# Kernel tuning notes

Measured on AMD Instinct MI355X. Metric: run time of the kernel, lower is better.

## Reference

```python
import jax, jax.numpy as jnp
import numpy as np

B, N, D, H = 4, 4096, 1024, 16
DH = D // H            # 64
GH = 4 * DH            # gate hidden = 256
FREQ = N // 2 + 1      # 2049
INV_SQRT2 = 0.7071067811865476


def _ln(x, g, b, eps=1e-6):
    mu = jnp.mean(x, axis=-1, keepdims=True)
    var = jnp.mean((x - mu) ** 2, axis=-1, keepdims=True)
    return (x - mu) / jnp.sqrt(var + eps) * g + b


def _xavier(k, out_f, in_f, gain=0.8):
    bound = gain * (6.0 / (in_f + out_f)) ** 0.5
    return jax.random.uniform(k, (out_f, in_f), jnp.float32, -bound, bound)


def setup_inputs() -> dict:
    key = jax.random.key(0)
    ks = jax.random.split(key, 8)
    return {
        'x': jax.random.normal(ks[0], (B, N, D), jnp.float32),
        'Wq': _xavier(ks[1], D, D),
        'Wv': _xavier(ks[2], D, D),
        'Wo': _xavier(ks[3], D, D),
        'ln_g': jnp.ones((DH,), jnp.float32),
        'ln_b': jnp.zeros((DH,), jnp.float32),
        'Wgup': _xavier(ks[4], GH, DH),
        'Wgdn': _xavier(ks[5], 2 * FREQ, GH),
        'Wwup': _xavier(ks[6], GH, DH),
        'Wwdn': _xavier(ks[7], N, GH),
    }


def reference(x, Wq, Wv, Wo, ln_g, ln_b, Wgup, Wgdn, Wwup, Wwdn):
    Bx, Nx, Dx = x.shape
    # projections -> [B, H, N, DH]
    q = (x @ Wq.T).reshape(Bx, Nx, H, DH).transpose(0, 2, 1, 3)
    v = (x @ Wv.T).reshape(Bx, Nx, H, DH).transpose(0, 2, 1, 3)
    # per-head summary token -> complex spectral gate over FREQ bins
    bar = _ln(q.mean(axis=2), ln_g, ln_b)                    # [B, H, DH]
    gr = (jax.nn.silu(bar @ Wgup.T) @ Wgdn.T)               # [B, H, 2*FREQ]
    gr = gr.reshape(Bx, H, FREQ, 2)
    gate = jax.lax.complex(gr[..., 0], gr[..., 1])           # [B, H, FREQ]
    # spectral mixing (chunk == seq_len, power-of-two path)
    spec = jnp.fft.rfft(v, axis=2, norm='ortho') * gate[..., None]
    v_t = jnp.fft.irfft(spec, n=Nx, axis=2, norm='ortho')    # [B, H, N, DH]
    # Haar wavelet refinement
    even, odd = v_t[..., ::2, :], v_t[..., 1::2, :]
    w = jnp.concatenate([even + odd, even - odd], axis=-2) * INV_SQRT2
    s = (jax.nn.silu(bar @ Wwup.T) @ Wwdn.T)[..., None]      # [B, H, N, 1]
    w = w * s
    half = Nx // 2
    low, high = w[..., :half, :], w[..., half:, :]
    # interleave even/odd back along seq dim
    refine = jnp.stack([low + high, low - high], axis=-2).reshape(Bx, H, Nx, DH) * INV_SQRT2
    v_t = v_t + refine
    y = v_t.transpose(0, 2, 1, 3).reshape(Bx, Nx, Dx)
    return y @ Wo.T
```

## Files before the change

### kernel.cpp

```cpp
#include <hip/hip_runtime.h>

constexpr int CB = 4, CN = 4096, CD = 1024, CH = 16, CDH = 64, CGH = 256, CFREQ = 2049, CBH = 64;

constexpr size_t OFF_XSUM = 0;
constexpr size_t OFF_HG   = 4096;
constexpr size_t OFF_HW   = OFF_HG + (size_t)CBH * CGH;
constexpr size_t OFF_GATE = OFF_HW + (size_t)CBH * CGH;
constexpr size_t OFF_S    = OFF_GATE + (size_t)CBH * 2 * CFREQ;
constexpr size_t OFF_CA   = OFF_S + (size_t)CBH * CN;
constexpr size_t OFF_CD   = OFF_CA + (size_t)CBH * (CN / 2);
constexpr size_t OFF_TW   = OFF_CD + (size_t)CBH * (CN / 2);
constexpr size_t OFF_VCOL = OFF_TW + 8192;
constexpr size_t OFF_XHI  = OFF_VCOL + (size_t)CB * CD * CN;
constexpr size_t OFF_XLO  = OFF_XHI + (size_t)CB * CN * CD / 2;
constexpr size_t OFF_WVHI = OFF_XLO + (size_t)CB * CN * CD / 2;
constexpr size_t OFF_WVLO = OFF_WVHI + (size_t)CD * CD / 2;
constexpr size_t OFF_WOHI = OFF_WVLO + (size_t)CD * CD / 2;
constexpr size_t OFF_WOLO = OFF_WOHI + (size_t)CD * CD / 2;

typedef __bf16 bf16x8 __attribute__((ext_vector_type(8)));
typedef __bf16 bf16x4 __attribute__((ext_vector_type(4)));
typedef float  f32x4  __attribute__((ext_vector_type(4)));
typedef float  f32x16 __attribute__((ext_vector_type(16)));

__device__ __forceinline__ float silu_f(float x) { return x / (1.0f + expf(-x)); }

__device__ __forceinline__ void gload16(const void* g, void* l) {
    __builtin_amdgcn_global_load_lds(
        reinterpret_cast<const __attribute__((address_space(1))) unsigned int*>(
            reinterpret_cast<uintptr_t>(g)),
        reinterpret_cast<__attribute__((address_space(3))) unsigned int*>(
            reinterpret_cast<uintptr_t>(l)),
        16, 0, 0);
}

__device__ __forceinline__ float2 cadd(float2 a, float2 b) { return make_float2(a.x + b.x, a.y + b.y); }
__device__ __forceinline__ float2 csub(float2 a, float2 b) { return make_float2(a.x - b.x, a.y - b.y); }
__device__ __forceinline__ float2 cmul(float2 a, float2 b) { return make_float2(a.x * b.x - a.y * b.y, a.x * b.y + a.y * b.x); }
__device__ __forceinline__ float2 cmulc(float2 a, float2 b) { return make_float2(a.x * b.x + a.y * b.y, a.y * b.x - a.x * b.y); }
__device__ __forceinline__ float2 mulni(float2 a) { return make_float2(a.y, -a.x); }
__device__ __forceinline__ float2 mulpi(float2 a) { return make_float2(-a.y, a.x); }

__device__ __forceinline__ int P(int r) { return r + (r >> 3); }

__device__ __forceinline__ int drev8(int k) {
    return ((k & 7) << 9) | (((k >> 3) & 7) << 6) | (((k >> 6) & 7) << 3) | ((k >> 9) & 7);
}

__device__ __forceinline__ void dft8_fwd(const float2 a[8], float2 A[8]) {
    float2 t0 = cadd(a[0], a[4]), t1 = csub(a[0], a[4]);
    float2 t2 = cadd(a[2], a[6]), t3 = mulni(csub(a[2], a[6]));
    float2 t4 = cadd(a[1], a[5]), t5 = csub(a[1], a[5]);
    float2 t6 = cadd(a[3], a[7]), t7 = mulni(csub(a[3], a[7]));
    float2 u0 = cadd(t0, t2), u1 = csub(t0, t2);
    float2 u2 = cadd(t1, t3), u3 = csub(t1, t3);
    float2 u4 = cadd(t4, t6), u5 = mulni(csub(t4, t6));
    float2 u6 = cadd(t5, t7), u7 = csub(t5, t7);
    const float s = 0.70710678118654752f;
    float2 w6 = make_float2(s * (u6.x + u6.y), s * (u6.y - u6.x));
    float2 w7 = make_float2(s * (u7.y - u7.x), -s * (u7.x + u7.y));
    A[0] = cadd(u0, u4); A[4] = csub(u0, u4);
    A[2] = cadd(u1, u5); A[6] = csub(u1, u5);
    A[1] = cadd(u2, w6); A[5] = csub(u2, w6);
    A[3] = cadd(u3, w7); A[7] = csub(u3, w7);
}

__device__ __forceinline__ void dft8_inv(const float2 a[8], float2 A[8]) {
    float2 t0 = cadd(a[0], a[4]), t1 = csub(a[0], a[4]);
    float2 t2 = cadd(a[2], a[6]), t3 = mulpi(csub(a[2], a[6]));
    float2 t4 = cadd(a[1], a[5]), t5 = csub(a[1], a[5]);
    float2 t6 = cadd(a[3], a[7]), t7 = mulpi(csub(a[3], a[7]));
    float2 u0 = cadd(t0, t2), u1 = csub(t0, t2);
    float2 u2 = cadd(t1, t3), u3 = csub(t1, t3);
    float2 u4 = cadd(t4, t6), u5 = mulpi(csub(t4, t6));
    float2 u6 = cadd(t5, t7), u7 = csub(t5, t7);
    const float s = 0.70710678118654752f;
    float2 w6 = make_float2(s * (u6.x - u6.y), s * (u6.x + u6.y));
    float2 w7 = make_float2(-s * (u7.x + u7.y), s * (u7.x - u7.y));
    A[0] = cadd(u0, u4); A[4] = csub(u0, u4);
    A[2] = cadd(u1, u5); A[6] = csub(u1, u5);
    A[1] = cadd(u2, w6); A[5] = csub(u2, w6);
    A[3] = cadd(u3, w7); A[7] = csub(u3, w7);
}

template <int M>
__device__ __forceinline__ void fwd_stage(float2* buf, const float2* __restrict__ tw, int t) {
    int j = t & (M - 1);
    int i0 = ((t & ~(M - 1)) << 3) + j;
    constexpr int TS = 512 / M;
    float2 a[8], A[8];
#pragma unroll
    for (int c = 0; c < 8; ++c) a[c] = buf[P(i0 + c * M)];
    dft8_fwd(a, A);
#pragma unroll
    for (int p = 0; p < 8; ++p) {
        float2 v = (M > 1 && p) ? cmul(A[p], tw[j * p * TS]) : A[p];
        buf[P(i0 + p * M)] = v;
    }
}

template <int M>
__device__ __forceinline__ void inv_stage(float2* buf, const float2* __restrict__ tw, int t) {
    int j = t & (M - 1);
    int i0 = ((t & ~(M - 1)) << 3) + j;
    constexpr int TS = 512 / M;
    float2 a[8], A[8];
#pragma unroll
    for (int c = 0; c < 8; ++c) {
        float2 v = buf[P(i0 + c * M)];
        a[c] = (M > 1 && c) ? cmulc(v, tw[j * c * TS]) : v;
    }
    dft8_inv(a, A);
#pragma unroll
    for (int p = 0; p < 8; ++p) buf[P(i0 + p * M)] = A[p];
}

__global__ void k_tw(float* twf) {
    int i = blockIdx.x * 256 + threadIdx.x;
    if (i < 4096) {
        double ang = -2.0 * 3.14159265358979323846 * (double)i / 4096.0;
        twf[2 * i]     = (float)cos(ang);
        twf[2 * i + 1] = (float)sin(ang);
    }
}

__global__ __launch_bounds__(256) void k_grev(const float* __restrict__ gateB,
                                              float2* __restrict__ grev) {
    int bh = blockIdx.y;
    int r = blockIdx.x * 256 + threadIdx.x;
    int k = drev8(r);
    const float2* g2 = (const float2*)gateB + (size_t)bh * CFREQ;
    float2 g;
    if (k <= 2048) g = g2[k];
    else { float2 gg = g2[4096 - k]; g = make_float2(gg.x, -gg.y); }
    grev[(size_t)bh * 4096 + r] = g;
}

__global__ __launch_bounds__(256) void k_meansplit(const float* __restrict__ X, float* __restrict__ xsum,
                                                   __bf16* __restrict__ hi, __bf16* __restrict__ lo) {
    int b = blockIdx.y;
    int c = blockIdx.x;
    int t = threadIdx.x;
    int half = t >> 7;
    int col = (t & 127) * 8;
    size_t base = (size_t)b * CN * CD + ((size_t)c * 64 + half * 32) * CD + col;
    float acc[8];
#pragma unroll
    for (int j = 0; j < 8; ++j) acc[j] = 0.f;
    for (int n = 0; n < 32; ++n) {
        size_t o = base + (size_t)n * CD;
        float4 v0 = *(const float4*)(X + o);
        float4 v1 = *(const float4*)(X + o + 4);
        float vv[8] = {v0.x, v0.y, v0.z, v0.w, v1.x, v1.y, v1.z, v1.w};
        bf16x8 hv, lv;
#pragma unroll
        for (int j = 0; j < 8; ++j) {
            acc[j] += vv[j];
            __bf16 h = (__bf16)vv[j];
            hv[j] = h;
            lv[j] = (__bf16)(vv[j] - (float)h);
        }
        *(bf16x8*)&hi[o] = hv;
        *(bf16x8*)&lo[o] = lv;
    }
#pragma unroll
    for (int j = 0; j < 8; ++j) atomicAdd(&xsum[b * CD + col + j], acc[j]);
}

__global__ __launch_bounds__(256) void k_barhidden(const float* __restrict__ xsum,
                                                   const float* __restrict__ Wq,
                                                   const float* __restrict__ ln_g,
                                                   const float* __restrict__ ln_b,
                                                   const float* __restrict__ Wgup,
                                                   const float* __restrict__ Wwup,
                                                   float* __restrict__ hg, float* __restrict__ hw) {
    int bh = blockIdx.x;
    int b = bh >> 4, h = bh & 15;
    int t = threadIdx.x;
    __shared__ float part[256];
    __shared__ float bar_s[64];
    int dh = t >> 2, seg = t & 3;
    const float* wrow = Wq + (size_t)(h * 64 + dh) * CD + seg * 256;
    const float* xs = xsum + b * CD + seg * 256;
    float acc = 0.f;
    for (int i = 0; i < 256; i += 4) {
        float4 w4 = *(const float4*)(wrow + i);
        float4 x4 = *(const float4*)(xs + i);
        acc += w4.x * x4.x + w4.y * x4.y + w4.z * x4.z + w4.w * x4.w;
    }
    part[t] = acc;
    __syncthreads();
    if (t < 64) {
        float q = (part[4 * t] + part[4 * t + 1] + part[4 * t + 2] + part[4 * t + 3]) * (1.0f / 4096.0f);
        float mu = q;
        for (int o = 32; o >= 1; o >>= 1) mu += __shfl_xor(mu, o, 64);
        mu *= (1.0f / 64.0f);
        float dev = q - mu;
        float vv = dev * dev;
        for (int o = 32; o >= 1; o >>= 1) vv += __shfl_xor(vv, o, 64);
        vv *= (1.0f / 64.0f);
        bar_s[t] = dev / sqrtf(vv + 1e-6f) * ln_g[t] + ln_b[t];
    }
    __syncthreads();
    const float* gup = Wgup + (size_t)t * CDH;
    const float* wup = Wwup + (size_t)t * CDH;
    float ag = 0.f, aw = 0.f;
    for (int i = 0; i < CDH; i += 4) {
        float4 bb = *(const float4*)(&bar_s[i]);
        float4 g4 = *(const float4*)(gup + i);
        float4 w4 = *(const float4*)(wup + i);
        ag += g4.x * bb.x + g4.y * bb.y + g4.z * bb.z + g4.w * bb.w;
        aw += w4.x * bb.x + w4.y * bb.y + w4.z * bb.z + w4.w * bb.w;
    }
    hg[bh * CGH + t] = silu_f(ag);
    hw[bh * CGH + t] = silu_f(aw);
}

__global__ __launch_bounds__(256) void k_gategemv(const float* __restrict__ Wgdn,
                                                  const float* __restrict__ Wwdn,
                                                  const float* __restrict__ hg,
                                                  const float* __restrict__ hw,
                                                  float* __restrict__ gate, float* __restrict__ sbuf) {
    int z = blockIdx.z;
    const float* Wd = z ? Wwdn : Wgdn;
    const float* hid = z ? hw : hg;
    float* out = z ? sbuf : gate;
    int Kout = z ? CN : 2 * CFREQ;
    int bh0 = blockIdx.y * 8;
    int t = threadIdx.x;
    int k = blockIdx.x * 256 + t;
    __shared__ float Lh[8][256];
    for (int g = 0; g < 8; ++g) Lh[g][t] = hid[(size_t)(bh0 + g) * CGH + t];
    __syncthreads();
    if (k >= Kout) return;
    float accv[8] = {0.f, 0.f, 0.f, 0.f, 0.f, 0.f, 0.f, 0.f};
    const float* wrow = Wd + (size_t)k * CGH;
    for (int j4 = 0; j4 < 64; ++j4) {
        float4 wv = *(const float4*)(wrow + 4 * j4);
#pragma unroll
        for (int g = 0; g < 8; ++g) {
            accv[g] += wv.x * Lh[g][4 * j4] + wv.y * Lh[g][4 * j4 + 1] +
                       wv.z * Lh[g][4 * j4 + 2] + wv.w * Lh[g][4 * j4 + 3];
        }
    }
    for (int g = 0; g < 8; ++g) out[(size_t)(bh0 + g) * Kout + k] = accv[g];
}

__global__ __launch_bounds__(256) void k_coef(const float* __restrict__ sbuf,
                                              float* __restrict__ ca, float* __restrict__ cd) {
    int bh = blockIdx.y;
    int i = blockIdx.x * 256 + threadIdx.x;
    float s0 = sbuf[(size_t)bh * CN + i];
    float s1 = sbuf[(size_t)bh * CN + 2048 + i];
    ca[(size_t)bh * 2048 + i] = 1.0f + 0.5f * (s0 + s1);
    cd[(size_t)bh * 2048 + i] = 0.5f * (s0 - s1);
}

__global__ __launch_bounds__(256) void k_split(const float* __restrict__ src,
                                               __bf16* __restrict__ hi, __bf16* __restrict__ lo,
                                               int n4) {
    int i = blockIdx.x * 256 + threadIdx.x;
    int stride = gridDim.x * 256;
    for (; i < n4; i += stride) {
        float4 v = ((const float4*)src)[i];
        __bf16 h0 = (__bf16)v.x, h1 = (__bf16)v.y, h2 = (__bf16)v.z, h3 = (__bf16)v.w;
        bf16x4 hv = {h0, h1, h2, h3};
        bf16x4 lv = {(__bf16)(v.x - (float)h0), (__bf16)(v.y - (float)h1),
                     (__bf16)(v.z - (float)h2), (__bf16)(v.w - (float)h3)};
        *(bf16x4*)&hi[4 * (size_t)i] = hv;
        *(bf16x4*)&lo[4 * (size_t)i] = lv;
    }
}

__global__ __launch_bounds__(256) void k_tsplit(const float* __restrict__ Vcol,
                                                __bf16* __restrict__ hi, __bf16* __restrict__ lo) {
    __shared__ float tile[32][33];
    int bx = blockIdx.x;
    int by = blockIdx.y;
    int b  = blockIdx.z;
    int t = threadIdx.x;
    int d = t >> 3, n4 = (t & 7) * 4;
    const float* src = Vcol + ((size_t)b * CD + by * 32 + d) * CN + bx * 32 + n4;
    float4 v = *(const float4*)src;
    tile[d][n4] = v.x; tile[d][n4 + 1] = v.y; tile[d][n4 + 2] = v.z; tile[d][n4 + 3] = v.w;
    __syncthreads();
    int n = t >> 3, d4 = (t & 7) * 4;
    size_t o = ((size_t)b * CN + bx * 32 + n) * CD + by * 32 + d4;
    float x0 = tile[d4][n], x1 = tile[d4 + 1][n], x2 = tile[d4 + 2][n], x3 = tile[d4 + 3][n];
    __bf16 h0 = (__bf16)x0, h1 = (__bf16)x1, h2 = (__bf16)x2, h3 = (__bf16)x3;
    bf16x4 hv = {h0, h1, h2, h3};
    bf16x4 lv = {(__bf16)(x0 - (float)h0), (__bf16)(x1 - (float)h1),
                 (__bf16)(x2 - (float)h2), (__bf16)(x3 - (float)h3)};
    *(bf16x4*)&hi[o] = hv;
    *(bf16x4*)&lo[o] = lv;
}

template <int TRANS>
__global__ __launch_bounds__(256, 1) void k_mfma_gemm(const __bf16* __restrict__ Ahi,
                                                      const __bf16* __restrict__ Alo,
                                                      const __bf16* __restrict__ Bhi,
                                                      const __bf16* __restrict__ Blo,
                                                      float* __restrict__ C) {
    __shared__ __align__(16) __bf16 lds[2][4][256 * 32];
    int t = threadIdx.x;
    int l = t & 63, w = t >> 6;
    int wm = w >> 1, wn = w & 1;
    int hw = blockIdx.x;
    int xcd = hw & 7, slot = hw >> 3;
    int m0 = (xcd * 8 + (slot >> 2)) * 256;
    int n0 = (slot & 3) * 256;

    const __bf16* gsrc = (w == 0) ? Ahi : (w == 1) ? Alo : (w == 2) ? Bhi : Blo;
    int gr0 = (w < 2) ? m0 : n0;
    unsigned o[16];
    int rl0[16];
#pragma unroll
    for (int i = 0; i < 16; ++i) {
        int rl = i * 16 + (l >> 2);
        unsigned sq = (unsigned)((l & 3) ^ ((rl >> 2) & 3));
        o[i] = (unsigned)(gr0 + rl) * 1024u + sq * 8u;
        rl0[i] = i * 16;
    }

    f32x16 acc[4][4];
#pragma unroll
    for (int mi = 0; mi < 4; ++mi)
#pragma unroll
        for (int ni = 0; ni < 4; ++ni)
#pragma unroll
            for (int q = 0; q < 16; ++q) acc[mi][ni][q] = 0.f;

#pragma unroll
    for (int i = 0; i < 16; ++i)
        gload16(gsrc + (size_t)o[i], &lds[0][w][rl0[i] * 32]);
    __syncthreads();

#pragma unroll 1
    for (int t32 = 0; t32 < 32; ++t32) {
        const int cur = t32 & 1;
        const size_t koff = (size_t)(t32 + 1) * 32;
        const bool pf = (t32 + 1) < 32;

        if (pf) {
#pragma unroll
            for (int i = 0; i < 16; ++i)
                gload16(gsrc + ((size_t)o[i] + koff), &lds[cur ^ 1][w][rl0[i] * 32]);
        }

        bf16x8 bfr[4][2][2];
#pragma unroll
        for (int ni = 0; ni < 4; ++ni) {
            int bcol = wn * 128 + ni * 32 + (l & 31);
            int bkey = (bcol >> 2) & 3;
#pragma unroll
            for (int s = 0; s < 2; ++s) {
                int sl = ((l >> 5) + 2 * s) ^ bkey;
                bfr[ni][s][0] = *(const bf16x8*)&lds[cur][2][bcol * 32 + sl * 8];
                bfr[ni][s][1] = *(const bf16x8*)&lds[cur][3][bcol * 32 + sl * 8];
            }
        }
        bf16x8 af[2][2];
        {
            int arow = wm * 128 + (l & 31);
            int akey = (arow >> 2) & 3;
            int sl = (l >> 5) ^ akey;
            af[0][0] = *(const bf16x8*)&lds[cur][0][arow * 32 + sl * 8];
            af[0][1] = *(const bf16x8*)&lds[cur][1][arow * 32 + sl * 8];
        }

#pragma unroll
        for (int u = 0; u < 8; ++u) {
            const int p = u >> 1, s = u & 1;
            if (u < 7) {
                const int un = u + 1, pn = un >> 1, sn = un & 1;
                int arow = wm * 128 + pn * 32 + (l & 31);
                int akey = (arow >> 2) & 3;
                int sl = ((l >> 5) + 2 * sn) ^ akey;
                af[(u + 1) & 1][0] = *(const bf16x8*)&lds[cur][0][arow * 32 + sl * 8];
                af[(u + 1) & 1][1] = *(const bf16x8*)&lds[cur][1][arow * 32 + sl * 8];
            }
#pragma unroll
            for (int ni = 0; ni < 4; ++ni) {
                acc[p][ni] = __builtin_amdgcn_mfma_f32_32x32x16_bf16(af[u & 1][0], bfr[ni][s][0], acc[p][ni], 0, 0, 0);
                acc[p][ni] = __builtin_amdgcn_mfma_f32_32x32x16_bf16(af[u & 1][0], bfr[ni][s][1], acc[p][ni], 0, 0, 0);
                acc[p][ni] = __builtin_amdgcn_mfma_f32_32x32x16_bf16(af[u & 1][1], bfr[ni][s][0], acc[p][ni], 0, 0, 0);
            }
        }
        __syncthreads();
    }

    if (TRANS) {
        int b = m0 >> 12;
        int tokb = (m0 & 4095) + wm * 128;
#pragma unroll
        for (int mi = 0; mi < 4; ++mi)
#pragma unroll
            for (int ni = 0; ni < 4; ++ni) {
                int dcol = n0 + wn * 128 + ni * 32 + (l & 31);
                float* base = C + ((size_t)(b * CD + dcol)) * CN;
#pragma unroll
                for (int q = 0; q < 4; ++q) {
                    int tok = tokb + mi * 32 + 8 * q + 4 * (l >> 5);
                    f32x4 v = {acc[mi][ni][4 * q], acc[mi][ni][4 * q + 1],
                               acc[mi][ni][4 * q + 2], acc[mi][ni][4 * q + 3]};
                    *(f32x4*)&base[tok] = v;
                }
            }
    } else {
#pragma unroll
        for (int mi = 0; mi < 4; ++mi)
#pragma unroll
            for (int ni = 0; ni < 4; ++ni) {
                int cc = n0 + wn * 128 + ni * 32 + (l & 31);
#pragma unroll
                for (int q = 0; q < 4; ++q) {
                    int r0 = m0 + wm * 128 + mi * 32 + 8 * q + 4 * (l >> 5);
#pragma unroll
                    for (int j = 0; j < 4; ++j)
                        C[(size_t)(r0 + j) * CD + cc] = acc[mi][ni][4 * q + j];
                }
            }
    }
}

__global__ __launch_bounds__(512, 2) void k_fft(float* __restrict__ Vcol,
                                                const float2* __restrict__ grevB,
                                                const float* __restrict__ caB,
                                                const float* __restrict__ cdB,
                                                const float2* __restrict__ tw) {
    __shared__ float2 buf[4608];
    int blk = blockIdx.x;
    int bh = blk >> 5, pr = blk & 31;
    int t = threadIdx.x;
    float* colA = Vcol + (size_t)(bh * 64 + pr * 2) * CN;
    float* colB = colA + CN;

    {
        float2 a[8], A[8];
#pragma unroll
        for (int c = 0; c < 8; ++c) {
            int n = t + 512 * c;
            a[c] = make_float2(colA[n], colB[n]);
        }
        dft8_fwd(a, A);
#pragma unroll
        for (int p = 0; p < 8; ++p) {
            float2 v = p ? cmul(A[p], tw[t * p]) : A[p];
            buf[P(t + 512 * p)] = v;
        }
    }
    __syncthreads();
    fwd_stage<64>(buf, tw, t);  __syncthreads();
    fwd_stage<8>(buf, tw, t);   __syncthreads();

    {
        const float2* gr = grevB + (size_t)bh * 4096 + (t << 3);
        int i0 = t << 3;
        float2 a[8], A[8];
#pragma unroll
        for (int c = 0; c < 8; ++c) a[c] = buf[P(i0 + c)];
        dft8_fwd(a, A);
#pragma unroll
        for (int p = 0; p < 8; ++p) A[p] = cmul(gr[p], A[p]);
        dft8_inv(A, a);
#pragma unroll
        for (int p = 0; p < 8; ++p) buf[P(i0 + p)] = a[p];
    }
    __syncthreads();

    inv_stage<8>(buf, tw, t);   __syncthreads();
    inv_stage<64>(buf, tw, t);  __syncthreads();

    {
        float2 a[8], A[8];
#pragma unroll
        for (int c = 0; c < 8; ++c) {
            float2 v = buf[P(t + 512 * c)];
            a[c] = c ? cmulc(v, tw[t * c]) : v;
        }
        dft8_inv(a, A);
        const float scale = 1.0f / 4096.0f;
        const float* ca = caB + (size_t)bh * 2048;
        const float* cd = cdB + (size_t)bh * 2048;
#pragma unroll
        for (int p = 0; p < 8; ++p) {
            int n = t + 512 * p;
            int i = n >> 1;
            float A_ = ca[i] * scale, D_ = cd[i] * scale;
            float ox = __shfl_xor(A[p].x, 1, 64);
            float oy = __shfl_xor(A[p].y, 1, 64);
            colA[n] = A_ * A[p].x + D_ * ox;
            colB[n] = A_ * A[p].y + D_ * oy;
        }
    }
}

extern "C" void kernel_launch(void* const* d_in, const int* in_sizes, int n_in,
                              void* d_out, int out_size, void* d_ws, size_t ws_size,
                              hipStream_t stream) {
    const float* x    = (const float*)d_in[0];
    const float* Wq   = (const float*)d_in[1];
    const float* Wv   = (const float*)d_in[2];
    const float* Wo   = (const float*)d_in[3];
    const float* ln_g = (const float*)d_in[4];
    const float* ln_b = (const float*)d_in[5];
    const float* Wgup = (const float*)d_in[6];
    const float* Wgdn = (const float*)d_in[7];
    const float* Wwup = (const float*)d_in[8];
    const float* Wwdn = (const float*)d_in[9];
    float* ws  = (float*)d_ws;
    float* out = (float*)d_out;

    __bf16* xhi  = (__bf16*)(ws + OFF_XHI);
    __bf16* xlo  = (__bf16*)(ws + OFF_XLO);
    __bf16* wvhi = (__bf16*)(ws + OFF_WVHI);
    __bf16* wvlo = (__bf16*)(ws + OFF_WVLO);
    __bf16* wohi = (__bf16*)(ws + OFF_WOHI);
    __bf16* wolo = (__bf16*)(ws + OFF_WOLO);
    __bf16* v2hi = (__bf16*)(ws + OFF_XHI);
    __bf16* v2lo = (__bf16*)(ws + OFF_XLO);
    float2* grev = (float2*)(ws + OFF_WVHI);

    hipMemsetAsync(ws + OFF_XSUM, 0, 4096 * sizeof(float), stream);
    k_tw<<<16, 256, 0, stream>>>(ws + OFF_TW);
    k_meansplit<<<dim3(64, 4), 256, 0, stream>>>(x, ws + OFF_XSUM, xhi, xlo);
    k_barhidden<<<64, 256, 0, stream>>>(ws + OFF_XSUM, Wq, ln_g, ln_b, Wgup, Wwup,
                                        ws + OFF_HG, ws + OFF_HW);
    k_gategemv<<<dim3(17, 8, 2), 256, 0, stream>>>(Wgdn, Wwdn, ws + OFF_HG, ws + OFF_HW,
                                                   ws + OFF_GATE, ws + OFF_S);
    k_coef<<<dim3(8, 64), 256, 0, stream>>>(ws + OFF_S, ws + OFF_CA, ws + OFF_CD);

    k_split<<<1024, 256, 0, stream>>>(Wv, wvhi, wvlo, CD * CD / 4);
    k_split<<<1024, 256, 0, stream>>>(Wo, wohi, wolo, CD * CD / 4);

    k_mfma_gemm<1><<<256, 256, 0, stream>>>(xhi, xlo, wvhi, wvlo, ws + OFF_VCOL);

    k_grev<<<dim3(16, 64), 256, 0, stream>>>(ws + OFF_GATE, grev);

    k_fft<<<2048, 512, 0, stream>>>(ws + OFF_VCOL, grev, ws + OFF_CA, ws + OFF_CD,
                                    (const float2*)(ws + OFF_TW));

    k_tsplit<<<dim3(128, 32, 4), 256, 0, stream>>>(ws + OFF_VCOL, v2hi, v2lo);

    k_mfma_gemm<0><<<256, 256, 0, stream>>>(v2hi, v2lo, wohi, wolo, out);
}
```

Baseline: 391.5 us.

## Fuse x bf16 hi/lo split into first GEMM's load path and merge small kernels

```diff
diff --git a/kernel.cpp b/kernel.cpp
--- a/kernel.cpp
+++ b/kernel.cpp
@@ -136,8 +136,7 @@
     grev[(size_t)bh * 4096 + r] = g;
 }
 
-__global__ __launch_bounds__(256) void k_meansplit(const float* __restrict__ X, float* __restrict__ xsum,
-                                                   __bf16* __restrict__ hi, __bf16* __restrict__ lo) {
+__global__ __launch_bounds__(256) void k_mean(const float* __restrict__ X, float* __restrict__ xsum) {
     int b = blockIdx.y;
     int c = blockIdx.x;
     int t = threadIdx.x;
@@ -151,17 +150,8 @@
         size_t o = base + (size_t)n * CD;
         float4 v0 = *(const float4*)(X + o);
         float4 v1 = *(const float4*)(X + o + 4);
-        float vv[8] = {v0.x, v0.y, v0.z, v0.w, v1.x, v1.y, v1.z, v1.w};
-        bf16x8 hv, lv;
-#pragma unroll
-        for (int j = 0; j < 8; ++j) {
-            acc[j] += vv[j];
-            __bf16 h = (__bf16)vv[j];
-            hv[j] = h;
-            lv[j] = (__bf16)(vv[j] - (float)h);
-        }
-        *(bf16x8*)&hi[o] = hv;
-        *(bf16x8*)&lo[o] = lv;
+        acc[0] += v0.x; acc[1] += v0.y; acc[2] += v0.z; acc[3] += v0.w;
+        acc[4] += v1.x; acc[5] += v1.y; acc[6] += v1.z; acc[7] += v1.w;
     }
 #pragma unroll
     for (int j = 0; j < 8; ++j) atomicAdd(&xsum[b * CD + col + j], acc[j]);
@@ -219,57 +209,70 @@
 __global__ __launch_bounds__(256) void k_gategemv(const float* __restrict__ Wgdn,
                                                   const float* __restrict__ Wwdn,
                                                   const float* __restrict__ hg,
-                                                  const float* __restrict__ hw,
-                                                  float* __restrict__ gate, float* __restrict__ sbuf) {
+                                                  const float* __restrict__ hw_,
+                                                  float* __restrict__ gate,
+                                                  float* __restrict__ ca, float* __restrict__ cd) {
     int z = blockIdx.z;
-    const float* Wd = z ? Wwdn : Wgdn;
-    const float* hid = z ? hw : hg;
-    float* out = z ? sbuf : gate;
-    int Kout = z ? CN : 2 * CFREQ;
+    if (z == 1 && blockIdx.x >= 8) return;
     int bh0 = blockIdx.y * 8;
     int t = threadIdx.x;
-    int k = blockIdx.x * 256 + t;
     __shared__ float Lh[8][256];
+    const float* hid = z ? hw_ : hg;
     for (int g = 0; g < 8; ++g) Lh[g][t] = hid[(size_t)(bh0 + g) * CGH + t];
     __syncthreads();
-    if (k >= Kout) return;
-    float accv[8] = {0.f, 0.f, 0.f, 0.f, 0.f, 0.f, 0.f, 0.f};
-    const float* wrow = Wd + (size_t)k * CGH;
-    for (int j4 = 0; j4 < 64; ++j4) {
-        float4 wv = *(const float4*)(wrow + 4 * j4);
-#pragma unroll
+    if (z == 0) {
+        int k = blockIdx.x * 256 + t;
+        if (k >= 2 * CFREQ) return;
+        float accv[8] = {0.f, 0.f, 0.f, 0.f, 0.f, 0.f, 0.f, 0.f};
+        const float* wrow = Wgdn + (size_t)k * CGH;
+        for (int j4 = 0; j4 < 64; ++j4) {
+            float4 wv = *(const float4*)(wrow + 4 * j4);
+#pragma unroll
+            for (int g = 0; g < 8; ++g) {
+                accv[g] += wv.x * Lh[g][4 * j4] + wv.y * Lh[g][4 * j4 + 1] +
+                           wv.z * Lh[g][4 * j4 + 2] + wv.w * Lh[g][4 * j4 + 3];
+            }
+        }
+        for (int g = 0; g < 8; ++g) gate[(size_t)(bh0 + g) * 2 * CFREQ + k] = accv[g];
+    } else {
+        int k = blockIdx.x * 256 + t;
+        float a0[8] = {0.f, 0.f, 0.f, 0.f, 0.f, 0.f, 0.f, 0.f};
+        float a1[8] = {0.f, 0.f, 0.f, 0.f, 0.f, 0.f, 0.f, 0.f};
+        const float* w0 = Wwdn + (size_t)k * CGH;
+        const float* w1 = Wwdn + (size_t)(k + 2048) * CGH;
+        for (int j4 = 0; j4 < 64; ++j4) {
+            float4 v0 = *(const float4*)(w0 + 4 * j4);
+            float4 v1 = *(const float4*)(w1 + 4 * j4);
+#pragma unroll
+            for (int g = 0; g < 8; ++g) {
+                float h0 = Lh[g][4 * j4], h1 = Lh[g][4 * j4 + 1], h2 = Lh[g][4 * j4 + 2], h3 = Lh[g][4 * j4 + 3];
+                a0[g] += v0.x * h0 + v0.y * h1 + v0.z * h2 + v0.w * h3;
+                a1[g] += v1.x * h0 + v1.y * h1 + v1.z * h2 + v1.w * h3;
+            }
+        }
         for (int g = 0; g < 8; ++g) {
-            accv[g] += wv.x * Lh[g][4 * j4] + wv.y * Lh[g][4 * j4 + 1] +
-                       wv.z * Lh[g][4 * j4 + 2] + wv.w * Lh[g][4 * j4 + 3];
-        }
-    }
-    for (int g = 0; g < 8; ++g) out[(size_t)(bh0 + g) * Kout + k] = accv[g];
-}
-
-__global__ __launch_bounds__(256) void k_coef(const float* __restrict__ sbuf,
-                                              float* __restrict__ ca, float* __restrict__ cd) {
-    int bh = blockIdx.y;
-    int i = blockIdx.x * 256 + threadIdx.x;
-    float s0 = sbuf[(size_t)bh * CN + i];
-    float s1 = sbuf[(size_t)bh * CN + 2048 + i];
-    ca[(size_t)bh * 2048 + i] = 1.0f + 0.5f * (s0 + s1);
-    cd[(size_t)bh * 2048 + i] = 0.5f * (s0 - s1);
-}
-
-__global__ __launch_bounds__(256) void k_split(const float* __restrict__ src,
-                                               __bf16* __restrict__ hi, __bf16* __restrict__ lo,
-                                               int n4) {
-    int i = blockIdx.x * 256 + threadIdx.x;
-    int stride = gridDim.x * 256;
-    for (; i < n4; i += stride) {
-        float4 v = ((const float4*)src)[i];
-        __bf16 h0 = (__bf16)v.x, h1 = (__bf16)v.y, h2 = (__bf16)v.z, h3 = (__bf16)v.w;
-        bf16x4 hv = {h0, h1, h2, h3};
-        bf16x4 lv = {(__bf16)(v.x - (float)h0), (__bf16)(v.y - (float)h1),
-                     (__bf16)(v.z - (float)h2), (__bf16)(v.w - (float)h3)};
-        *(bf16x4*)&hi[4 * (size_t)i] = hv;
-        *(bf16x4*)&lo[4 * (size_t)i] = lv;
-    }
+            float s0 = a0[g], s1 = a1[g];
+            ca[(size_t)(bh0 + g) * 2048 + k] = 1.0f + 0.5f * (s0 + s1);
+            cd[(size_t)(bh0 + g) * 2048 + k] = 0.5f * (s0 - s1);
+        }
+    }
+}
+
+__global__ __launch_bounds__(256) void k_split2(const float* __restrict__ Wv, const float* __restrict__ Wo,
+                                                __bf16* __restrict__ wvhi, __bf16* __restrict__ wvlo,
+                                                __bf16* __restrict__ wohi, __bf16* __restrict__ wolo) {
+    int b = blockIdx.x;
+    const float* src = (b < 1024) ? Wv : Wo;
+    __bf16* hi = (b < 1024) ? wvhi : wohi;
+    __bf16* lo = (b < 1024) ? wvlo : wolo;
+    int i = (b & 1023) * 256 + threadIdx.x;
+    float4 v = ((const float4*)src)[i];
+    __bf16 h0 = (__bf16)v.x, h1 = (__bf16)v.y, h2 = (__bf16)v.z, h3 = (__bf16)v.w;
+    bf16x4 hv = {h0, h1, h2, h3};
+    bf16x4 lv = {(__bf16)(v.x - (float)h0), (__bf16)(v.y - (float)h1),
+                 (__bf16)(v.z - (float)h2), (__bf16)(v.w - (float)h3)};
+    *(bf16x4*)&hi[4 * (size_t)i] = hv;
+    *(bf16x4*)&lo[4 * (size_t)i] = lv;
 }
 
 __global__ __launch_bounds__(256) void k_tsplit(const float* __restrict__ Vcol,
@@ -295,7 +298,150 @@
     *(bf16x4*)&lo[o] = lv;
 }
 
-template <int TRANS>
+__global__ __launch_bounds__(256, 1) void k_gemm1_x(const float* __restrict__ X,
+                                                    const __bf16* __restrict__ BhiP,
+                                                    const __bf16* __restrict__ BloP,
+                                                    float* __restrict__ C) {
+    __shared__ __align__(16) __bf16 lds[2][4][256 * 32];
+    int t = threadIdx.x;
+    int l = t & 63, w = t >> 6;
+    int wm = w >> 1, wn = w & 1;
+    int hw = blockIdx.x;
+    int xcd = hw & 7, slot = hw >> 3;
+    int m0 = (xcd * 8 + (slot >> 2)) * 256;
+    int n0 = (slot & 3) * 256;
+
+    const __bf16* gsrcB = (w < 2) ? BhiP : BloP;
+    const int bplane = 2 + (w >> 1);
+    unsigned ob[8];
+    int rb[8];
+#pragma unroll
+    for (int i = 0; i < 8; ++i) {
+        int rl = (w & 1) * 128 + i * 16 + (l >> 2);
+        unsigned sq = (unsigned)((l & 3) ^ ((rl >> 2) & 3));
+        ob[i] = (unsigned)(n0 + rl) * 1024u + sq * 8u;
+        rb[i] = (w & 1) * 128 + i * 16;
+    }
+
+    const int arow_t = t >> 3;
+    const int acol = (t & 7) * 4;
+
+    f32x16 acc[4][4];
+#pragma unroll
+    for (int mi = 0; mi < 4; ++mi)
+#pragma unroll
+        for (int ni = 0; ni < 4; ++ni)
+#pragma unroll
+            for (int q = 0; q < 16; ++q) acc[mi][ni][q] = 0.f;
+
+#pragma unroll
+    for (int i = 0; i < 8; ++i)
+        gload16(gsrcB + (size_t)ob[i], &lds[0][bplane][rb[i] * 32]);
+#pragma unroll
+    for (int i = 0; i < 8; ++i) {
+        int arow = i * 32 + arow_t;
+        float4 v = *(const float4*)(X + (size_t)(m0 + arow) * 1024 + acol);
+        __bf16 h0 = (__bf16)v.x, h1 = (__bf16)v.y, h2 = (__bf16)v.z, h3 = (__bf16)v.w;
+        bf16x4 hv = {h0, h1, h2, h3};
+        bf16x4 lv = {(__bf16)(v.x - (float)h0), (__bf16)(v.y - (float)h1),
+                     (__bf16)(v.z - (float)h2), (__bf16)(v.w - (float)h3)};
+        int sl = (acol >> 3) ^ ((arow >> 2) & 3);
+        *(bf16x4*)&lds[0][0][arow * 32 + sl * 8 + (acol & 4)] = hv;
+        *(bf16x4*)&lds[0][1][arow * 32 + sl * 8 + (acol & 4)] = lv;
+    }
+    __syncthreads();
+
+#pragma unroll 1
+    for (int t32 = 0; t32 < 32; ++t32) {
+        const int cur = t32 & 1;
+        const int koff = (t32 + 1) * 32;
+        const bool pf = (t32 + 1) < 32;
+
+        float4 xr[8];
+        if (pf) {
+#pragma unroll
+            for (int i = 0; i < 8; ++i)
+                gload16(gsrcB + ((size_t)ob[i] + koff), &lds[cur ^ 1][bplane][rb[i] * 32]);
+#pragma unroll
+            for (int i = 0; i < 8; ++i)
+                xr[i] = *(const float4*)(X + (size_t)(m0 + i * 32 + arow_t) * 1024 + koff + acol);
+        }
+
+        bf16x8 bfr[4][2][2];
+#pragma unroll
+        for (int ni = 0; ni < 4; ++ni) {
+            int bcol = wn * 128 + ni * 32 + (l & 31);
+            int bkey = (bcol >> 2) & 3;
+#pragma unroll
+            for (int s = 0; s < 2; ++s) {
+                int sl = ((l >> 5) + 2 * s) ^ bkey;
+                bfr[ni][s][0] = *(const bf16x8*)&lds[cur][2][bcol * 32 + sl * 8];
+                bfr[ni][s][1] = *(const bf16x8*)&lds[cur][3][bcol * 32 + sl * 8];
+            }
+        }
+        bf16x8 af[2][2];
+        {
+            int arow = wm * 128 + (l & 31);
+            int akey = (arow >> 2) & 3;
+            int sl = (l >> 5) ^ akey;
+            af[0][0] = *(const bf16x8*)&lds[cur][0][arow * 32 + sl * 8];
+            af[0][1] = *(const bf16x8*)&lds[cur][1][arow * 32 + sl * 8];
+        }
+
+#pragma unroll
+        for (int u = 0; u < 8; ++u) {
+            const int p = u >> 1, s = u & 1;
+            if (u < 7) {
+                const int un = u + 1, pn = un >> 1, sn = un & 1;
+                int arow = wm * 128 + pn * 32 + (l & 31);
+                int akey = (arow >> 2) & 3;
+                int sl = ((l >> 5) + 2 * sn) ^ akey;
+                af[(u + 1) & 1][0] = *(const bf16x8*)&lds[cur][0][arow * 32 + sl * 8];
+                af[(u + 1) & 1][1] = *(const bf16x8*)&lds[cur][1][arow * 32 + sl * 8];
+            }
+#pragma unroll
+            for (int ni = 0; ni < 4; ++ni) {
+                acc[p][ni] = __builtin_amdgcn_mfma_f32_32x32x16_bf16(af[u & 1][0], bfr[ni][s][0], acc[p][ni], 0, 0, 0);
+                acc[p][ni] = __builtin_amdgcn_mfma_f32_32x32x16_bf16(af[u & 1][0], bfr[ni][s][1], acc[p][ni], 0, 0, 0);
+                acc[p][ni] = __builtin_amdgcn_mfma_f32_32x32x16_bf16(af[u & 1][1], bfr[ni][s][0], acc[p][ni], 0, 0, 0);
+            }
+        }
+
+        if (pf) {
+#pragma unroll
+            for (int i = 0; i < 8; ++i) {
+                float4 v = xr[i];
+                int arow = i * 32 + arow_t;
+                __bf16 h0 = (__bf16)v.x, h1 = (__bf16)v.y, h2 = (__bf16)v.z, h3 = (__bf16)v.w;
+                bf16x4 hv = {h0, h1, h2, h3};
+                bf16x4 lv = {(__bf16)(v.x - (float)h0), (__bf16)(v.y - (float)h1),
+                             (__bf16)(v.z - (float)h2), (__bf16)(v.w - (float)h3)};
+                int sl = (acol >> 3) ^ ((arow >> 2) & 3);
+                *(bf16x4*)&lds[cur ^ 1][0][arow * 32 + sl * 8 + (acol & 4)] = hv;
+                *(bf16x4*)&lds[cur ^ 1][1][arow * 32 + sl * 8 + (acol & 4)] = lv;
+            }
+        }
+        __syncthreads();
+    }
+
+    int b = m0 >> 12;
+    int tokb = (m0 & 4095) + wm * 128;
+#pragma unroll
+    for (int mi = 0; mi < 4; ++mi)
+#pragma unroll
+        for (int ni = 0; ni < 4; ++ni) {
+            int dcol = n0 + wn * 128 + ni * 32 + (l & 31);
+            float* base = C + ((size_t)(b * CD + dcol)) * CN;
+#pragma unroll
+            for (int q = 0; q < 4; ++q) {
+                int tok = tokb + mi * 32 + 8 * q + 4 * (l >> 5);
+                f32x4 v = {acc[mi][ni][4 * q], acc[mi][ni][4 * q + 1],
+                           acc[mi][ni][4 * q + 2], acc[mi][ni][4 * q + 3]};
+                *(f32x4*)&base[tok] = v;
+            }
+        }
+}
+
 __global__ __launch_bounds__(256, 1) void k_mfma_gemm(const __bf16* __restrict__ Ahi,
                                                       const __bf16* __restrict__ Alo,
                                                       const __bf16* __restrict__ Bhi,
@@ -389,38 +535,19 @@
         __syncthreads();
     }
 
-    if (TRANS) {
-        int b = m0 >> 12;
-        int tokb = (m0 & 4095) + wm * 128;
-#pragma unroll
-        for (int mi = 0; mi < 4; ++mi)
-#pragma unroll
-            for (int ni = 0; ni < 4; ++ni) {
-                int dcol = n0 + wn * 128 + ni * 32 + (l & 31);
-                float* base = C + ((size_t)(b * CD + dcol)) * CN;
-#pragma unroll
-                for (int q = 0; q < 4; ++q) {
-                    int tok = tokb + mi * 32 + 8 * q + 4 * (l >> 5);
-                    f32x4 v = {acc[mi][ni][4 * q], acc[mi][ni][4 * q + 1],
-                               acc[mi][ni][4 * q + 2], acc[mi][ni][4 * q + 3]};
-                    *(f32x4*)&base[tok] = v;
-                }
-            }
-    } else {
-#pragma unroll
-        for (int mi = 0; mi < 4; ++mi)
-#pragma unroll
-            for (int ni = 0; ni < 4; ++ni) {
-                int cc = n0 + wn * 128 + ni * 32 + (l & 31);
-#pragma unroll
-                for (int q = 0; q < 4; ++q) {
-                    int r0 = m0 + wm * 128 + mi * 32 + 8 * q + 4 * (l >> 5);
-#pragma unroll
-                    for (int j = 0; j < 4; ++j)
-                        C[(size_t)(r0 + j) * CD + cc] = acc[mi][ni][4 * q + j];
-                }
-            }
-    }
+#pragma unroll
+    for (int mi = 0; mi < 4; ++mi)
+#pragma unroll
+        for (int ni = 0; ni < 4; ++ni) {
+            int cc = n0 + wn * 128 + ni * 32 + (l & 31);
+#pragma unroll
+            for (int q = 0; q < 4; ++q) {
+                int r0 = m0 + wm * 128 + mi * 32 + 8 * q + 4 * (l >> 5);
+#pragma unroll
+                for (int j = 0; j < 4; ++j)
+                    C[(size_t)(r0 + j) * CD + cc] = acc[mi][ni][4 * q + j];
+            }
+        }
 }
 
 __global__ __launch_bounds__(512, 2) void k_fft(float* __restrict__ Vcol,
@@ -511,8 +638,6 @@
     float* ws  = (float*)d_ws;
     float* out = (float*)d_out;
 
-    __bf16* xhi  = (__bf16*)(ws + OFF_XHI);
-    __bf16* xlo  = (__bf16*)(ws + OFF_XLO);
     __bf16* wvhi = (__bf16*)(ws + OFF_WVHI);
     __bf16* wvlo = (__bf16*)(ws + OFF_WVLO);
     __bf16* wohi = (__bf16*)(ws + OFF_WOHI);
@@ -523,17 +648,15 @@
 
     hipMemsetAsync(ws + OFF_XSUM, 0, 4096 * sizeof(float), stream);
     k_tw<<<16, 256, 0, stream>>>(ws + OFF_TW);
-    k_meansplit<<<dim3(64, 4), 256, 0, stream>>>(x, ws + OFF_XSUM, xhi, xlo);
+    k_mean<<<dim3(64, 4), 256, 0, stream>>>(x, ws + OFF_XSUM);
     k_barhidden<<<64, 256, 0, stream>>>(ws + OFF_XSUM, Wq, ln_g, ln_b, Wgup, Wwup,
                                         ws + OFF_HG, ws + OFF_HW);
     k_gategemv<<<dim3(17, 8, 2), 256, 0, stream>>>(Wgdn, Wwdn, ws + OFF_HG, ws + OFF_HW,
-                                                   ws + OFF_GATE, ws + OFF_S);
-    k_coef<<<dim3(8, 64), 256, 0, stream>>>(ws + OFF_S, ws + OFF_CA, ws + OFF_CD);
-
-    k_split<<<1024, 256, 0, stream>>>(Wv, wvhi, wvlo, CD * CD / 4);
-    k_split<<<1024, 256, 0, stream>>>(Wo, wohi, wolo, CD * CD / 4);
-
-    k_mfma_gemm<1><<<256, 256, 0, stream>>>(xhi, xlo, wvhi, wvlo, ws + OFF_VCOL);
+                                                   ws + OFF_GATE, ws + OFF_CA, ws + OFF_CD);
+
+    k_split2<<<2048, 256, 0, stream>>>(Wv, Wo, wvhi, wvlo, wohi, wolo);
+
+    k_gemm1_x<<<256, 256, 0, stream>>>(x, wvhi, wvlo, ws + OFF_VCOL);
 
     k_grev<<<dim3(16, 64), 256, 0, stream>>>(ws + OFF_GATE, grev);
 
@@ -542,5 +665,5 @@
 
     k_tsplit<<<dim3(128, 32, 4), 256, 0, stream>>>(ws + OFF_VCOL, v2hi, v2lo);
 
-    k_mfma_gemm<0><<<256, 256, 0, stream>>>(v2hi, v2lo, wohi, wolo, out);
-}
+    k_mfma_gemm<<<256, 256, 0, stream>>>(v2hi, v2lo, wohi, wolo, out);
+}
```

New measurement: 401.8 us. +2.6%, slower.

## Pre-pack weight fragments for direct global MFMA loads; fuse coef into gate GEMV

Applied to the files above, without the earlier changes.

```diff
diff --git a/kernel.cpp b/kernel.cpp
--- a/kernel.cpp
+++ b/kernel.cpp
@@ -219,57 +219,72 @@
 __global__ __launch_bounds__(256) void k_gategemv(const float* __restrict__ Wgdn,
                                                   const float* __restrict__ Wwdn,
                                                   const float* __restrict__ hg,
-                                                  const float* __restrict__ hw,
-                                                  float* __restrict__ gate, float* __restrict__ sbuf) {
+                                                  const float* __restrict__ hw_,
+                                                  float* __restrict__ gate,
+                                                  float* __restrict__ ca, float* __restrict__ cd) {
     int z = blockIdx.z;
-    const float* Wd = z ? Wwdn : Wgdn;
-    const float* hid = z ? hw : hg;
-    float* out = z ? sbuf : gate;
-    int Kout = z ? CN : 2 * CFREQ;
+    if (z == 1 && blockIdx.x >= 8) return;
     int bh0 = blockIdx.y * 8;
     int t = threadIdx.x;
-    int k = blockIdx.x * 256 + t;
     __shared__ float Lh[8][256];
+    const float* hid = z ? hw_ : hg;
     for (int g = 0; g < 8; ++g) Lh[g][t] = hid[(size_t)(bh0 + g) * CGH + t];
     __syncthreads();
-    if (k >= Kout) return;
-    float accv[8] = {0.f, 0.f, 0.f, 0.f, 0.f, 0.f, 0.f, 0.f};
-    const float* wrow = Wd + (size_t)k * CGH;
-    for (int j4 = 0; j4 < 64; ++j4) {
-        float4 wv = *(const float4*)(wrow + 4 * j4);
-#pragma unroll
+    if (z == 0) {
+        int k = blockIdx.x * 256 + t;
+        if (k >= 2 * CFREQ) return;
+        float accv[8] = {0.f, 0.f, 0.f, 0.f, 0.f, 0.f, 0.f, 0.f};
+        const float* wrow = Wgdn + (size_t)k * CGH;
+        for (int j4 = 0; j4 < 64; ++j4) {
+            float4 wv = *(const float4*)(wrow + 4 * j4);
+#pragma unroll
+            for (int g = 0; g < 8; ++g) {
+                accv[g] += wv.x * Lh[g][4 * j4] + wv.y * Lh[g][4 * j4 + 1] +
+                           wv.z * Lh[g][4 * j4 + 2] + wv.w * Lh[g][4 * j4 + 3];
+            }
+        }
+        for (int g = 0; g < 8; ++g) gate[(size_t)(bh0 + g) * 2 * CFREQ + k] = accv[g];
+    } else {
+        int k = blockIdx.x * 256 + t;
+        float a0[8] = {0.f, 0.f, 0.f, 0.f, 0.f, 0.f, 0.f, 0.f};
+        float a1[8] = {0.f, 0.f, 0.f, 0.f, 0.f, 0.f, 0.f, 0.f};
+        const float* w0 = Wwdn + (size_t)k * CGH;
+        const float* w1 = Wwdn + (size_t)(k + 2048) * CGH;
+        for (int j4 = 0; j4 < 64; ++j4) {
+            float4 v0 = *(const float4*)(w0 + 4 * j4);
+            float4 v1 = *(const float4*)(w1 + 4 * j4);
+#pragma unroll
+            for (int g = 0; g < 8; ++g) {
+                float h0 = Lh[g][4 * j4], h1 = Lh[g][4 * j4 + 1], h2 = Lh[g][4 * j4 + 2], h3 = Lh[g][4 * j4 + 3];
+                a0[g] += v0.x * h0 + v0.y * h1 + v0.z * h2 + v0.w * h3;
+                a1[g] += v1.x * h0 + v1.y * h1 + v1.z * h2 + v1.w * h3;
+            }
+        }
         for (int g = 0; g < 8; ++g) {
-            accv[g] += wv.x * Lh[g][4 * j4] + wv.y * Lh[g][4 * j4 + 1] +
-                       wv.z * Lh[g][4 * j4 + 2] + wv.w * Lh[g][4 * j4 + 3];
-        }
-    }
-    for (int g = 0; g < 8; ++g) out[(size_t)(bh0 + g) * Kout + k] = accv[g];
-}
-
-__global__ __launch_bounds__(256) void k_coef(const float* __restrict__ sbuf,
-                                              float* __restrict__ ca, float* __restrict__ cd) {
-    int bh = blockIdx.y;
-    int i = blockIdx.x * 256 + threadIdx.x;
-    float s0 = sbuf[(size_t)bh * CN + i];
-    float s1 = sbuf[(size_t)bh * CN + 2048 + i];
-    ca[(size_t)bh * 2048 + i] = 1.0f + 0.5f * (s0 + s1);
-    cd[(size_t)bh * 2048 + i] = 0.5f * (s0 - s1);
-}
-
-__global__ __launch_bounds__(256) void k_split(const float* __restrict__ src,
-                                               __bf16* __restrict__ hi, __bf16* __restrict__ lo,
-                                               int n4) {
-    int i = blockIdx.x * 256 + threadIdx.x;
-    int stride = gridDim.x * 256;
-    for (; i < n4; i += stride) {
-        float4 v = ((const float4*)src)[i];
-        __bf16 h0 = (__bf16)v.x, h1 = (__bf16)v.y, h2 = (__bf16)v.z, h3 = (__bf16)v.w;
-        bf16x4 hv = {h0, h1, h2, h3};
-        bf16x4 lv = {(__bf16)(v.x - (float)h0), (__bf16)(v.y - (float)h1),
-                     (__bf16)(v.z - (float)h2), (__bf16)(v.w - (float)h3)};
-        *(bf16x4*)&hi[4 * (size_t)i] = hv;
-        *(bf16x4*)&lo[4 * (size_t)i] = lv;
-    }
+            float s0 = a0[g], s1 = a1[g];
+            ca[(size_t)(bh0 + g) * 2048 + k] = 1.0f + 0.5f * (s0 + s1);
+            cd[(size_t)(bh0 + g) * 2048 + k] = 0.5f * (s0 - s1);
+        }
+    }
+}
+
+__global__ __launch_bounds__(256) void k_splitpack(const float* __restrict__ Wv, const float* __restrict__ Wo,
+                                                   __bf16* __restrict__ wvhi, __bf16* __restrict__ wvlo,
+                                                   __bf16* __restrict__ wohi, __bf16* __restrict__ wolo) {
+    int b = blockIdx.x;
+    const float* src = (b < 1024) ? Wv : Wo;
+    __bf16* hi = (b < 1024) ? wvhi : wohi;
+    __bf16* lo = (b < 1024) ? wvlo : wolo;
+    int i = (b & 1023) * 256 + threadIdx.x;
+    int col = i >> 8, k0 = (i & 255) * 4;
+    float4 v = ((const float4*)src)[i];
+    __bf16 h0 = (__bf16)v.x, h1 = (__bf16)v.y, h2 = (__bf16)v.z, h3 = (__bf16)v.w;
+    bf16x4 hv = {h0, h1, h2, h3};
+    bf16x4 lv = {(__bf16)(v.x - (float)h0), (__bf16)(v.y - (float)h1),
+                 (__bf16)(v.z - (float)h2), (__bf16)(v.w - (float)h3)};
+    size_t flat = (((size_t)(col >> 5) * 64 + (k0 >> 4)) * 64 + (col & 31) + 32 * ((k0 >> 3) & 1)) * 8 + (k0 & 7);
+    *(bf16x4*)&hi[flat] = hv;
+    *(bf16x4*)&lo[flat] = lv;
 }
 
 __global__ __launch_bounds__(256) void k_tsplit(const float* __restrict__ Vcol,
@@ -298,10 +313,10 @@
 template <int TRANS>
 __global__ __launch_bounds__(256, 1) void k_mfma_gemm(const __bf16* __restrict__ Ahi,
                                                       const __bf16* __restrict__ Alo,
-                                                      const __bf16* __restrict__ Bhi,
-                                                      const __bf16* __restrict__ Blo,
+                                                      const __bf16* __restrict__ BpkHi,
+                                                      const __bf16* __restrict__ BpkLo,
                                                       float* __restrict__ C) {
-    __shared__ __align__(16) __bf16 lds[2][4][256 * 32];
+    __shared__ __align__(16) __bf16 lds[2][2][256 * 32];
     int t = threadIdx.x;
     int l = t & 63, w = t >> 6;
     int wm = w >> 1, wn = w & 1;
@@ -309,17 +324,19 @@
     int xcd = hw & 7, slot = hw >> 3;
     int m0 = (xcd * 8 + (slot >> 2)) * 256;
     int n0 = (slot & 3) * 256;
-
-    const __bf16* gsrc = (w == 0) ? Ahi : (w == 1) ? Alo : (w == 2) ? Bhi : Blo;
-    int gr0 = (w < 2) ? m0 : n0;
-    unsigned o[16];
-    int rl0[16];
-#pragma unroll
-    for (int i = 0; i < 16; ++i) {
-        int rl = i * 16 + (l >> 2);
+    int nb_base = (slot & 3) * 8 + wn * 4;
+
+    const __bf16* gsrcA = (w < 2) ? Ahi : Alo;
+    const int apl = w >> 1;
+    const int ahalf = w & 1;
+    unsigned o[8];
+    int rl0[8];
+#pragma unroll
+    for (int i = 0; i < 8; ++i) {
+        int rl = ahalf * 128 + i * 16 + (l >> 2);
         unsigned sq = (unsigned)((l & 3) ^ ((rl >> 2) & 3));
-        o[i] = (unsigned)(gr0 + rl) * 1024u + sq * 8u;
-        rl0[i] = i * 16;
+        o[i] = (unsigned)(m0 + rl) * 1024u + sq * 8u;
+        rl0[i] = ahalf * 128 + i * 16;
     }
 
     f32x16 acc[4][4];
@@ -331,8 +348,8 @@
             for (int q = 0; q < 16; ++q) acc[mi][ni][q] = 0.f;
 
 #pragma unroll
-    for (int i = 0; i < 16; ++i)
-        gload16(gsrc + (size_t)o[i], &lds[0][w][rl0[i] * 32]);
+    for (int i = 0; i < 8; ++i)
+        gload16(gsrcA + (size_t)o[i], &lds[0][apl][rl0[i] * 32]);
     __syncthreads();
 
 #pragma unroll 1
@@ -341,51 +358,46 @@
         const size_t koff = (size_t)(t32 + 1) * 32;
         const bool pf = (t32 + 1) < 32;
 
+        bf16x8 bfr[2][4][2];
+#pragma unroll
+        for (int s = 0; s < 2; ++s)
+#pragma unroll
+            for (int ni = 0; ni < 4; ++ni) {
+                size_t off = (((size_t)(nb_base + ni) * 64 + 2 * t32 + s) * 64 + l) * 8;
+                bfr[s][ni][0] = *(const bf16x8*)&BpkHi[off];
+                bfr[s][ni][1] = *(const bf16x8*)&BpkLo[off];
+            }
+
         if (pf) {
 #pragma unroll
-            for (int i = 0; i < 16; ++i)
-                gload16(gsrc + ((size_t)o[i] + koff), &lds[cur ^ 1][w][rl0[i] * 32]);
-        }
-
-        bf16x8 bfr[4][2][2];
-#pragma unroll
-        for (int ni = 0; ni < 4; ++ni) {
-            int bcol = wn * 128 + ni * 32 + (l & 31);
-            int bkey = (bcol >> 2) & 3;
-#pragma unroll
-            for (int s = 0; s < 2; ++s) {
-                int sl = ((l >> 5) + 2 * s) ^ bkey;
-                bfr[ni][s][0] = *(const bf16x8*)&lds[cur][2][bcol * 32 + sl * 8];
-                bfr[ni][s][1] = *(const bf16x8*)&lds[cur][3][bcol * 32 + sl * 8];
+            for (int i = 0; i < 8; ++i)
+                gload16(gsrcA + ((size_t)o[i] + koff), &lds[cur ^ 1][apl][rl0[i] * 32]);
+        }
+
+        bf16x8 afr[2][4][2];
+#pragma unroll
+        for (int s = 0; s < 2; ++s)
+#pragma unroll
+            for (int p = 0; p < 4; ++p) {
+                int arow = wm * 128 + p * 32 + (l & 31);
+                int akey = (arow >> 2) & 3;
+                int sl = ((l >> 5) + 2 * s) ^ akey;
+                afr[s][p][0] = *(const bf16x8*)&lds[cur][0][arow * 32 + sl * 8];
+                afr[s][p][1] = *(const bf16x8*)&lds[cur][1][arow * 32 + sl * 8];
             }
-        }
-        bf16x8 af[2][2];
-        {
-            int arow = wm * 128 + (l & 31);
-            int akey = (arow >> 2) & 3;
-            int sl = (l >> 5) ^ akey;
-            af[0][0] = *(const bf16x8*)&lds[cur][0][arow * 32 + sl * 8];
-            af[0][1] = *(const bf16x8*)&lds[cur][1][arow * 32 + sl * 8];
-        }
-
-#pragma unroll
-        for (int u = 0; u < 8; ++u) {
-            const int p = u >> 1, s = u & 1;
-            if (u < 7) {
-                const int un = u + 1, pn = un >> 1, sn = un & 1;
-                int arow = wm * 128 + pn * 32 + (l & 31);
-                int akey = (arow >> 2) & 3;
-                int sl = ((l >> 5) + 2 * sn) ^ akey;
-                af[(u + 1) & 1][0] = *(const bf16x8*)&lds[cur][0][arow * 32 + sl * 8];
-                af[(u + 1) & 1][1] = *(const bf16x8*)&lds[cur][1][arow * 32 + sl * 8];
-            }
-#pragma unroll
-            for (int ni = 0; ni < 4; ++ni) {
-                acc[p][ni] = __builtin_amdgcn_mfma_f32_32x32x16_bf16(af[u & 1][0], bfr[ni][s][0], acc[p][ni], 0, 0, 0);
-                acc[p][ni] = __builtin_amdgcn_mfma_f32_32x32x16_bf16(af[u & 1][0], bfr[ni][s][1], acc[p][ni], 0, 0, 0);
-                acc[p][ni] = __builtin_amdgcn_mfma_f32_32x32x16_bf16(af[u & 1][1], bfr[ni][s][0], acc[p][ni], 0, 0, 0);
-            }
-        }
+
+#pragma unroll
+        for (int s = 0; s < 2; ++s)
+#pragma unroll
+            for (int pass = 0; pass < 3; ++pass)
+#pragma unroll
+                for (int p = 0; p < 4; ++p)
+#pragma unroll
+                    for (int ni = 0; ni < 4; ++ni) {
+                        bf16x8 a = (pass < 2) ? afr[s][p][0] : afr[s][p][1];
+                        bf16x8 bb = (pass == 1) ? bfr[s][ni][1] : bfr[s][ni][0];
+                        acc[p][ni] = __builtin_amdgcn_mfma_f32_32x32x16_bf16(a, bb, acc[p][ni], 0, 0, 0);
+                    }
         __syncthreads();
     }
 
@@ -527,11 +539,9 @@
     k_barhidden<<<64, 256, 0, stream>>>(ws + OFF_XSUM, Wq, ln_g, ln_b, Wgup, Wwup,
                                         ws + OFF_HG, ws + OFF_HW);
     k_gategemv<<<dim3(17, 8, 2), 256, 0, stream>>>(Wgdn, Wwdn, ws + OFF_HG, ws + OFF_HW,
-                                                   ws + OFF_GATE, ws + OFF_S);
-    k_coef<<<dim3(8, 64), 256, 0, stream>>>(ws + OFF_S, ws + OFF_CA, ws + OFF_CD);
-
-    k_split<<<1024, 256, 0, stream>>>(Wv, wvhi, wvlo, CD * CD / 4);
-    k_split<<<1024, 256, 0, stream>>>(Wo, wohi, wolo, CD * CD / 4);
+                                                   ws + OFF_GATE, ws + OFF_CA, ws + OFF_CD);
+
+    k_splitpack<<<2048, 256, 0, stream>>>(Wv, Wo, wvhi, wvlo, wohi, wolo);
 
     k_mfma_gemm<1><<<256, 256, 0, stream>>>(xhi, xlo, wvhi, wvlo, ws + OFF_VCOL);
 
```

After: 413.9 us. +5.7%, slower.
